# Performance work log

Measured on AMD Instinct MI355X. Metric: run time of the kernel, lower is better.

The kernel has to match this reference:

```python
import jax, jax.numpy as jnp
import numpy as np

PI = np.pi


def _apply_1q(state, gate, wire, n):
    # state: [B, 2**n] complex64; gate: [2,2] (shared) or [B,2,2] (per-sample)
    # PennyLane convention: wire 0 is the most-significant bit of the state index.
    B = state.shape[0]
    left, right = 2 ** wire, 2 ** (n - wire - 1)
    s = state.reshape(B, left, 2, right)
    if gate.ndim == 2:
        s = jnp.einsum('kl,balr->bakr', gate, s)
    else:
        s = jnp.einsum('bkl,balr->bakr', gate, s)
    return s.reshape(B, -1)


def _apply_cz(state, wire, n):
    # CZ on (wire, wire+1): flip sign of |..11..> amplitudes
    B = state.shape[0]
    left, right = 2 ** wire, 2 ** (n - wire - 2)
    s = state.reshape(B, left, 2, 2, right)
    s = s.at[:, :, 1, 1, :].multiply(-1.0)
    return s.reshape(B, -1)


def _ry_batched(theta):
    # theta: [B] -> [B,2,2] complex RY(theta)
    h = 0.5 * theta
    c, s = jnp.cos(h), jnp.sin(h)
    g = jnp.stack([jnp.stack([c, -s], -1), jnp.stack([s, c], -1)], -2)
    return g.astype(jnp.complex64)


def _rot(phi, theta, omega):
    # Rot = RZ(omega) @ RY(theta) @ RZ(phi)
    c, s = jnp.cos(0.5 * theta), jnp.sin(0.5 * theta)
    e_mm = jnp.exp(-0.5j * (phi + omega))
    e_pm = jnp.exp(0.5j * (phi - omega))
    e_mp = jnp.exp(-0.5j * (phi - omega))
    e_pp = jnp.exp(0.5j * (phi + omega))
    g = jnp.stack([jnp.stack([e_mm * c, -e_pm * s]), jnp.stack([e_mp * s, e_pp * c])])
    return g.astype(jnp.complex64)


def _simulate(enc, weights):
    # enc: [B, n_qubits] in [-1,1]; weights: [n_layers, n_qubits, 3]
    n_layers, n, _ = weights.shape
    B = enc.shape[0]
    state = jnp.zeros((B, 2 ** n), jnp.complex64).at[:, 0].set(1.0)
    ry = [_ry_batched(enc[:, i] * PI) for i in range(n)]
    for l in range(n_layers):
        for i in range(n):
            state = _apply_1q(state, ry[i], i, n)
        for i in range(n):
            state = _apply_1q(state, _rot(weights[l, i, 0], weights[l, i, 1], weights[l, i, 2]), i, n)
        for i in range(n - 1):
            state = _apply_cz(state, i, n)
    for i in range(n):
        state = _apply_1q(state, ry[i], i, n)
    probs = state.real ** 2 + state.imag ** 2  # [B, 2**n]
    # <Z_i> = sum_k probs[k] * (-1)^bit_i(k), wire 0 = MSB
    bits = (jnp.arange(2 ** n)[None, :] >> (n - 1 - jnp.arange(n))[:, None]) & 1
    signs = (1 - 2 * bits).astype(probs.dtype)  # [n, 2**n]
    return probs @ signs.T  # [B, n]


def setup_inputs() -> dict:
    B, D, NQ, NL, NA = 32768, 16, 8, 4, 4
    key = jax.random.key(0)
    ks = jax.random.split(key, 6)

    def lin(k, o, i):
        b = 1.0 / np.sqrt(i)
        k1, k2 = jax.random.split(k)
        return (jax.random.uniform(k1, (o, i), jnp.float32, -b, b),
                jax.random.uniform(k2, (o,), jnp.float32, -b, b))

    enc_w1, enc_b1 = lin(ks[1], 8, D)
    enc_w2, enc_b2 = lin(ks[2], NQ, 8)
    dec_w1, dec_b1 = lin(ks[3], 8, NQ)
    dec_w2, dec_b2 = lin(ks[4], NA, 8)
    q_weights = jax.random.uniform(ks[5], (NL, NQ, 3), jnp.float32, 0.0, 2.0 * PI)
    x = jax.random.normal(ks[0], (B, D), jnp.float32)
    return {"x": x, "enc_w1": enc_w1, "enc_b1": enc_b1, "enc_w2": enc_w2, "enc_b2": enc_b2,
            "q_weights": q_weights, "dec_w1": dec_w1, "dec_b1": dec_b1, "dec_w2": dec_w2, "dec_b2": dec_b2}


def reference(x, enc_w1, enc_b1, enc_w2, enc_b2, q_weights, dec_w1, dec_b1, dec_w2, dec_b2):
    h = jax.nn.relu(x @ enc_w1.T + enc_b1)
    enc = jnp.tanh(h @ enc_w2.T + enc_b2)          # [B, n_qubits]
    q = _simulate(enc, q_weights)                  # [B, n_qubits] PauliZ expvals
    h2 = jax.nn.relu(q @ dec_w1.T + dec_b1)
    return h2 @ dec_w2.T + dec_b2                  # [B, n_actions]
```

## Files before the change

### kernel.cpp

```cpp
#include <hip/hip_runtime.h>
#include <math.h>


#define PI_F 3.14159265358979323846f

typedef float v2f __attribute__((ext_vector_type(2)));

struct C2 { float re, im; };
__device__ __forceinline__ C2 cmul(C2 a, C2 b) {
    C2 r;
    r.re = fmaf(a.re, b.re, -a.im * b.im);
    r.im = fmaf(a.re, b.im,  a.im * b.re);
    return r;
}
__device__ __forceinline__ float fxor(float x, int m) {
    return __int_as_float(__float_as_int(x) ^ m);
}

__device__ __forceinline__ v2f pk_fma(v2f a, v2f b, v2f c) {
    v2f d; asm("v_pk_fma_f32 %0, %1, %2, %3" : "=v"(d) : "v"(a), "v"(b), "v"(c)); return d;
}

__device__ __forceinline__ v2f mkbc(float c) { v2f r; r.x = c; return r; }

__device__ __forceinline__ v2f pk_mul_s(float c, v2f z) {
    v2f cb = mkbc(c), d;
    asm("v_pk_mul_f32 %0, %1, %2 op_sel_hi:[0,1]"
        : "=v"(d) : "v"(cb), "v"(z));
    return d;
}
__device__ __forceinline__ v2f pk_mul_neg_s(float c, v2f z) {
    v2f cb = mkbc(c), d;
    asm("v_pk_mul_f32 %0, %1, %2 op_sel_hi:[0,1] neg_lo:[1,0] neg_hi:[1,0]"
        : "=v"(d) : "v"(cb), "v"(z));
    return d;
}
__device__ __forceinline__ v2f pk_fma_s(float c, v2f b, v2f acc) {
    v2f cb = mkbc(c), d;
    asm("v_pk_fma_f32 %0, %1, %2, %3 op_sel_hi:[0,1,1]"
        : "=v"(d) : "v"(cb), "v"(b), "v"(acc));
    return d;
}
__device__ __forceinline__ v2f pk_fma_nn_s(float c, v2f b, v2f acc) {
    v2f cb = mkbc(c), d;
    asm("v_pk_fma_f32 %0, %1, %2, %3 op_sel_hi:[0,1,1] neg_lo:[1,0,0] neg_hi:[1,0,0]"
        : "=v"(d) : "v"(cb), "v"(b), "v"(acc));
    return d;
}
__device__ __forceinline__ v2f pk_fma_swl_s(float c, v2f z, v2f acc) {
    v2f cb = mkbc(c), d;
    asm("v_pk_fma_f32 %0, %1, %2, %3 op_sel:[0,1,0] op_sel_hi:[0,0,1] neg_lo:[1,0,0]"
        : "=v"(d) : "v"(cb), "v"(z), "v"(acc));
    return d;
}
__device__ __forceinline__ v2f pk_fma_swh_s(float c, v2f z, v2f acc) {
    v2f cb = mkbc(c), d;
    asm("v_pk_fma_f32 %0, %1, %2, %3 op_sel:[0,1,0] op_sel_hi:[0,0,1] neg_hi:[1,0,0]"
        : "=v"(d) : "v"(cb), "v"(z), "v"(acc));
    return d;
}
__device__ __forceinline__ v2f cmulv(v2f z, C2 c) {
    return pk_fma_swl_s(c.im, z, pk_mul_s(c.re, z));
}

template<int CTRL>
__device__ __forceinline__ float dppf(float x) {
    int xi = __float_as_int(x);
    int r = __builtin_amdgcn_update_dpp(xi, xi, CTRL, 0xF, 0xF, false);
    return __int_as_float(r);
}
template<int M>
__device__ __forceinline__ float lxor(float x) {
    if constexpr (M == 1)      return dppf<0xB1>(x);
    else if constexpr (M == 2) return dppf<0x4E>(x);
    else                       return dppf<0x128>(x);
}

__device__ __forceinline__ void load_G2(const float* __restrict__ c_lds, int g,
                                        float cc, float ss,
                                        float& ar, float& ai, float& br, float& bi) {
    const float4 c0 = *(const float4*)(c_lds + 4 * g);
    ar = fmaf(c0.x, cc, -c0.z * ss);
    ai = fmaf(c0.y, cc,  c0.w * ss);
    br = fmaf(c0.z, cc,  c0.x * ss);
    bi = fmaf(c0.w, cc, -c0.y * ss);
}

template<int M>
__device__ __forceinline__ void su2_cross(float cSr, float cSi, float cOr, float cOi,
                                          v2f z[32]) {
#pragma unroll
    for (int c = 0; c < 4; c++) {
        v2f p[8];
#pragma unroll
        for (int k = 0; k < 8; k++) {
            p[k].x = lxor<M>(z[c * 8 + k].x);
            p[k].y = lxor<M>(z[c * 8 + k].y);
        }
#pragma unroll
        for (int k = 0; k < 8; k++) {
            const int t = c * 8 + k;
            v2f n = pk_mul_s(cSr, z[t]);
            n = pk_fma_swl_s(cSi, z[t], n);
            n = pk_fma_s    (cOr, p[k], n);
            n = pk_fma_swl_s(cOi, p[k], n);
            z[t] = n;
        }
    }
}

template<int ST>
__device__ __forceinline__ void su2_inlane(float ar, float ai, float br, float bi,
                                           v2f z[32]) {
#pragma unroll
    for (int t = 0; t < 32; t++) {
        if ((t & ST) == 0) {
            const int u = t + ST;
            v2f x = z[t], y = z[u];
            v2f nx = pk_mul_s(ar, x);
            nx = pk_fma_swl_s(ai, x, nx);
            nx = pk_fma_nn_s (br, y, nx);
            nx = pk_fma_swl_s(bi, y, nx);
            v2f ny = pk_mul_s(br, x);
            ny = pk_fma_swl_s(bi, x, ny);
            ny = pk_fma_s    (ar, y, ny);
            ny = pk_fma_swh_s(ai, y, ny);
            z[t] = nx; z[u] = ny;
        }
    }
}

template<int M>
__device__ __forceinline__ v2f xcorr_cross(const v2f z[32]) {
    v2f acc = (v2f){0.0f, 0.0f};
#pragma unroll
    for (int c = 0; c < 4; c++) {
        v2f p[8];
#pragma unroll
        for (int k = 0; k < 8; k++) {
            p[k].x = lxor<M>(z[c * 8 + k].x);
            p[k].y = lxor<M>(z[c * 8 + k].y);
        }
#pragma unroll
        for (int k = 0; k < 8; k++) acc = pk_fma(z[c * 8 + k], p[k], acc);
    }
    return acc;
}
template<int ST>
__device__ __forceinline__ v2f xcorr_inlane(const v2f z[32]) {
    v2f acc = (v2f){0.0f, 0.0f};
#pragma unroll
    for (int t = 0; t < 32; t++)
        if ((t & ST) == 0) acc = pk_fma(z[t], z[t + ST], acc);
    return acc;
}

__host__ __device__ constexpr bool czt5(int t) {
    return ((((t >> 4) & (t >> 3)) ^ ((t >> 3) & (t >> 2)) ^
             ((t >> 2) & (t >> 1)) ^ ((t >> 1) & t)) & 1) != 0;
}

__global__ __launch_bounds__(128, 2) void qdqn_kernel(
    const float* __restrict__ x,
    const float* __restrict__ ew1, const float* __restrict__ eb1,
    const float* __restrict__ ew2, const float* __restrict__ eb2,
    const float* __restrict__ qw,
    const float* __restrict__ dw1, const float* __restrict__ db1,
    const float* __restrict__ dw2, const float* __restrict__ db2,
    float* __restrict__ out, int B, int NL) {
    __shared__ __align__(16) float c_lds[32 * 4];
    __shared__ __align__(16) float hx[2][8][8];
    __shared__ __align__(16) float csx[2][8][16];

    const int tid = threadIdx.x;
    const int wave = tid >> 6;
    const int lane = tid & 63;
    const int g = (lane & 3) | ((lane >> 1) & 4);
    const int grp = ((lane >> 2) & 1) | ((lane >> 3) & 6);
    int s = blockIdx.x * 16 + wave * 8 + grp;
    if (s >= B) s = B - 1;

    float xv[16];
    {
        const float4* xp = (const float4*)(x + s * 16);
#pragma unroll
        for (int i = 0; i < 4; i++) {
            float4 v = xp[i];
            xv[4*i] = v.x; xv[4*i+1] = v.y; xv[4*i+2] = v.z; xv[4*i+3] = v.w;
        }
    }

    const int n_gates = NL * 8;
    if (tid < n_gates) {
        const int gg = tid;
        float phi = qw[3 * gg + 0], th = qw[3 * gg + 1], om = qw[3 * gg + 2];
        float c = __cosf(0.5f * th), sv = __sinf(0.5f * th);
        float A = 0.5f * (phi + om), Bb = 0.5f * (phi - om);
        float* o = c_lds + 4 * gg;
        o[0] =  __cosf(A) * c;   o[1] = -__sinf(A) * c;
        o[2] =  __cosf(Bb) * sv; o[3] = -__sinf(Bb) * sv;
    }
    __syncthreads();

    float cq[8], sq[8];
    {
        float a = eb1[g];
#pragma unroll
        for (int i = 0; i < 16; i++) a = fmaf(ew1[g * 16 + i], xv[i], a);
        hx[wave][grp][g] = fmaxf(a, 0.0f);
        __builtin_amdgcn_wave_barrier();
        float4 h01 = *(const float4*)&hx[wave][grp][0];
        float4 h23 = *(const float4*)&hx[wave][grp][4];
        float b = eb2[g];
        b = fmaf(ew2[g*8+0], h01.x, b); b = fmaf(ew2[g*8+1], h01.y, b);
        b = fmaf(ew2[g*8+2], h01.z, b); b = fmaf(ew2[g*8+3], h01.w, b);
        b = fmaf(ew2[g*8+4], h23.x, b); b = fmaf(ew2[g*8+5], h23.y, b);
        b = fmaf(ew2[g*8+6], h23.z, b); b = fmaf(ew2[g*8+7], h23.w, b);
        float e = 1.0f - __fdividef(2.0f, __expf(2.0f * b) + 1.0f);
        float ang = e * (0.5f * PI_F);
        float2* cso = (float2*)&csx[wave][grp][2 * g];
        *cso = make_float2(__cosf(ang), __sinf(ang));
        __builtin_amdgcn_wave_barrier();
#pragma unroll
        for (int k = 0; k < 4; k++) {
            float4 v = *(const float4*)&csx[wave][grp][4 * k];
            cq[2*k] = v.x; sq[2*k] = v.y; cq[2*k+1] = v.z; sq[2*k+1] = v.w;
        }
    }

    int hiM[3], loM[3];
#pragma unroll
    for (int q = 0; q < 3; q++) {
        int hi = (g >> (2 - q)) & 1;
        hiM[q] = hi << 31;
        loM[q] = hiM[q] ^ 0x80000000;
    }

    const int g0b = g & 1, g1b = (g >> 1) & 1, g2b = (g >> 2) & 1;
    const float mLo = ((g2b & g1b) ^ (g1b & g0b)) ? -1.0f : 1.0f;
    const float mHi = g0b ? -mLo : mLo;

    v2f z[32];
    {
        C2 P; P.re = 1.0f; P.im = 0.0f;
        C2 A[5], Bc[5];
#pragma unroll
        for (int q = 0; q < 8; q++) {
            float ar, ai, br, bi;
            load_G2(c_lds, q, cq[q], sq[q], ar, ai, br, bi);
            if (q < 3) {
                const bool hi = (g >> (2 - q)) & 1;
                C2 f; f.re = hi ? br : ar; f.im = hi ? bi : ai;
                P = cmul(P, f);
            } else {
                A[q-3].re = ar;  A[q-3].im = ai;
                Bc[q-3].re = br; Bc[q-3].im = bi;
            }
        }
        z[0] = (v2f){P.re, P.im};
#pragma unroll
        for (int w = 0; w < 5; w++) {
            const int n = 1 << w;
#pragma unroll
            for (int i = n - 1; i >= 0; i--) {
                v2f v = z[i];
                z[2*i+1] = cmulv(v, Bc[w]);
                z[2*i]   = cmulv(v, A[w]);
            }
        }
#pragma unroll
        for (int t = 0; t < 32; t++) {
            const float m = (t < 16) ? mLo : mHi;
            z[t] = czt5(t) ? pk_mul_neg_s(m, z[t]) : pk_mul_s(m, z[t]);
        }
    }

    for (int l = 1; l < NL; l++) {
        const int gb = l * 8;
        float ar, ai, br, bi;
        load_G2(c_lds, gb+0, cq[0], sq[0], ar, ai, br, bi);
        su2_cross<8>(ar, fxor(ai,hiM[0]), fxor(br,loM[0]), bi, z);
        load_G2(c_lds, gb+1, cq[1], sq[1], ar, ai, br, bi);
        su2_cross<2>(ar, fxor(ai,hiM[1]), fxor(br,loM[1]), bi, z);
        load_G2(c_lds, gb+2, cq[2], sq[2], ar, ai, br, bi);
        su2_cross<1>(ar, fxor(ai,hiM[2]), fxor(br,loM[2]), bi, z);
        load_G2(c_lds, gb+3, cq[3], sq[3], ar, ai, br, bi);
        su2_inlane<16>(ar, ai, br, bi, z);
        load_G2(c_lds, gb+4, cq[4], sq[4], ar, ai, br, bi);
        su2_inlane<8>(ar, ai, br, bi, z);
        load_G2(c_lds, gb+5, cq[5], sq[5], ar, ai, br, bi);
        su2_inlane<4>(ar, ai, br, bi, z);
        load_G2(c_lds, gb+6, cq[6], sq[6], ar, ai, br, bi);
        su2_inlane<2>(ar, ai, br, bi, z);
        load_G2(c_lds, gb+7, cq[7], sq[7], ar, ai, br, bi);
        su2_inlane<1>(ar, ai, br, bi, z);
#pragma unroll
        for (int t = 0; t < 32; t++) {
            const float m = (t < 16) ? mLo : mHi;
            z[t] = czt5(t) ? pk_mul_neg_s(m, z[t]) : pk_mul_s(m, z[t]);
        }
    }

    v2f xa[8];
    xa[0] = xcorr_cross<8>(z);
    xa[1] = xcorr_cross<2>(z);
    xa[2] = xcorr_cross<1>(z);
    xa[3] = xcorr_inlane<16>(z);
    xa[4] = xcorr_inlane<8>(z);
    xa[5] = xcorr_inlane<4>(z);
    xa[6] = xcorr_inlane<2>(z);
    xa[7] = xcorr_inlane<1>(z);

    float p[32];
#pragma unroll
    for (int t = 0; t < 32; t++) p[t] = fmaf(z[t].x, z[t].x, z[t].y * z[t].y);

    float s16[16], zW[8];
    {
        float d = 0.0f;
#pragma unroll
        for (int i = 0; i < 16; i++) {
            s16[i] = p[2*i] + p[2*i+1];
            d += p[2*i] - p[2*i+1];
        }
        zW[7] = d;
        float s8[8]; d = 0.0f;
#pragma unroll
        for (int i = 0; i < 8; i++) {
            s8[i] = s16[2*i] + s16[2*i+1];
            d += s16[2*i] - s16[2*i+1];
        }
        zW[6] = d;
        float s4[4]; d = 0.0f;
#pragma unroll
        for (int i = 0; i < 4; i++) {
            s4[i] = s8[2*i] + s8[2*i+1];
            d += s8[2*i] - s8[2*i+1];
        }
        zW[5] = d;
        float s2a = s4[0] + s4[1], s2b = s4[2] + s4[3];
        zW[4] = (s4[0] - s4[1]) + (s4[2] - s4[3]);
        float sumP = s2a + s2b;
        zW[3] = s2a - s2b;
        zW[0] = g2b ? -sumP : sumP;
        zW[1] = g1b ? -sumP : sumP;
        zW[2] = g0b ? -sumP : sumP;
    }

#pragma unroll
    for (int w = 0; w < 8; w++) {
        const float c2 = fmaf(cq[w], cq[w], -sq[w] * sq[w]);
        const float cs = cq[w] * sq[w];
        const float s2 = (w < 3 ? 2.0f : 4.0f) * cs;
        zW[w] = fmaf(c2, zW[w], -s2 * (xa[w].x + xa[w].y));
    }

#pragma unroll
    for (int w = 0; w < 8; w++) zW[w] += lxor<1>(zW[w]);
#pragma unroll
    for (int w = 0; w < 8; w++) zW[w] += lxor<2>(zW[w]);
#pragma unroll
    for (int w = 0; w < 8; w++) zW[w] += lxor<8>(zW[w]);

    {
        float a = db1[g];
#pragma unroll
        for (int w = 0; w < 8; w++) a = fmaf(dw1[g * 8 + w], zW[w], a);
        hx[wave][grp][g] = fmaxf(a, 0.0f);
        __builtin_amdgcn_wave_barrier();
        float4 h01 = *(const float4*)&hx[wave][grp][0];
        float4 h23 = *(const float4*)&hx[wave][grp][4];
        const int o = g & 3;
        float acc = db2[o];
        acc = fmaf(dw2[o*8+0], h01.x, acc); acc = fmaf(dw2[o*8+1], h01.y, acc);
        acc = fmaf(dw2[o*8+2], h01.z, acc); acc = fmaf(dw2[o*8+3], h01.w, acc);
        acc = fmaf(dw2[o*8+4], h23.x, acc); acc = fmaf(dw2[o*8+5], h23.y, acc);
        acc = fmaf(dw2[o*8+6], h23.z, acc); acc = fmaf(dw2[o*8+7], h23.w, acc);
        out[s * 4 + o] = acc;
    }
}

extern "C" void kernel_launch(void* const* d_in, const int* in_sizes, int n_in,
                              void* d_out, int out_size, void* d_ws, size_t ws_size,
                              hipStream_t stream) {
    const float* x   = (const float*)d_in[0];
    const float* ew1 = (const float*)d_in[1];
    const float* eb1 = (const float*)d_in[2];
    const float* ew2 = (const float*)d_in[3];
    const float* eb2 = (const float*)d_in[4];
    const float* qw  = (const float*)d_in[5];
    const float* dw1 = (const float*)d_in[6];
    const float* db1 = (const float*)d_in[7];
    const float* dw2 = (const float*)d_in[8];
    const float* db2 = (const float*)d_in[9];
    float* out = (float*)d_out;

    int B = in_sizes[0] / 16;
    int n_gates = in_sizes[5] / 3;
    int NL = n_gates / 8;

    int blocks = (B + 15) / 16;
    qdqn_kernel<<<blocks, 128, 0, stream>>>(x, ew1, eb1, ew2, eb2, qw,
                                            dw1, db1, dw2, db2, out, B, NL);
}
```

Before: 116.8 us.

## Use single-wave blocks and batch-load per-layer gate coefficients from LDS

Blocks shrink from two waves to one, with eight samples per block, so the block-wide __syncthreads becomes a wave barrier and the shared arrays lose their wave dimension. Each layer's eight gate coefficient vectors are now read from LDS in one batch before the gate chain, instead of one read right before each gate, so LDS latency can overlap with arithmetic. The grid doubles and each block redoes the trig setup for the gate table, and holding the extra float4s raises register pressure.

```diff
diff --git a/kernel.cpp b/kernel.cpp
--- a/kernel.cpp
+++ b/kernel.cpp
@@ -76,10 +76,8 @@
     else                       return dppf<0x128>(x);
 }
 
-__device__ __forceinline__ void load_G2(const float* __restrict__ c_lds, int g,
-                                        float cc, float ss,
+__device__ __forceinline__ void make_G2(float4 c0, float cc, float ss,
                                         float& ar, float& ai, float& br, float& bi) {
-    const float4 c0 = *(const float4*)(c_lds + 4 * g);
     ar = fmaf(c0.x, cc, -c0.z * ss);
     ai = fmaf(c0.y, cc,  c0.w * ss);
     br = fmaf(c0.z, cc,  c0.x * ss);
@@ -160,7 +158,7 @@
              ((t >> 2) & (t >> 1)) ^ ((t >> 1) & t)) & 1) != 0;
 }
 
-__global__ __launch_bounds__(128, 2) void qdqn_kernel(
+__global__ __launch_bounds__(64, 2) void qdqn_kernel(
     const float* __restrict__ x,
     const float* __restrict__ ew1, const float* __restrict__ eb1,
     const float* __restrict__ ew2, const float* __restrict__ eb2,
@@ -169,15 +167,14 @@
     const float* __restrict__ dw2, const float* __restrict__ db2,
     float* __restrict__ out, int B, int NL) {
     __shared__ __align__(16) float c_lds[32 * 4];
-    __shared__ __align__(16) float hx[2][8][8];
-    __shared__ __align__(16) float csx[2][8][16];
+    __shared__ __align__(16) float hx[8][8];
+    __shared__ __align__(16) float csx[8][16];
 
     const int tid = threadIdx.x;
-    const int wave = tid >> 6;
-    const int lane = tid & 63;
+    const int lane = tid;
     const int g = (lane & 3) | ((lane >> 1) & 4);
     const int grp = ((lane >> 2) & 1) | ((lane >> 3) & 6);
-    int s = blockIdx.x * 16 + wave * 8 + grp;
+    int s = blockIdx.x * 8 + grp;
     if (s >= B) s = B - 1;
 
     float xv[16];
@@ -200,17 +197,17 @@
         o[0] =  __cosf(A) * c;   o[1] = -__sinf(A) * c;
         o[2] =  __cosf(Bb) * sv; o[3] = -__sinf(Bb) * sv;
     }
-    __syncthreads();
+    __builtin_amdgcn_wave_barrier();
 
     float cq[8], sq[8];
     {
         float a = eb1[g];
 #pragma unroll
         for (int i = 0; i < 16; i++) a = fmaf(ew1[g * 16 + i], xv[i], a);
-        hx[wave][grp][g] = fmaxf(a, 0.0f);
+        hx[grp][g] = fmaxf(a, 0.0f);
         __builtin_amdgcn_wave_barrier();
-        float4 h01 = *(const float4*)&hx[wave][grp][0];
-        float4 h23 = *(const float4*)&hx[wave][grp][4];
+        float4 h01 = *(const float4*)&hx[grp][0];
+        float4 h23 = *(const float4*)&hx[grp][4];
         float b = eb2[g];
         b = fmaf(ew2[g*8+0], h01.x, b); b = fmaf(ew2[g*8+1], h01.y, b);
         b = fmaf(ew2[g*8+2], h01.z, b); b = fmaf(ew2[g*8+3], h01.w, b);
@@ -218,12 +215,12 @@
         b = fmaf(ew2[g*8+6], h23.z, b); b = fmaf(ew2[g*8+7], h23.w, b);
         float e = 1.0f - __fdividef(2.0f, __expf(2.0f * b) + 1.0f);
         float ang = e * (0.5f * PI_F);
-        float2* cso = (float2*)&csx[wave][grp][2 * g];
+        float2* cso = (float2*)&csx[grp][2 * g];
         *cso = make_float2(__cosf(ang), __sinf(ang));
         __builtin_amdgcn_wave_barrier();
 #pragma unroll
         for (int k = 0; k < 4; k++) {
-            float4 v = *(const float4*)&csx[wave][grp][4 * k];
+            float4 v = *(const float4*)&csx[grp][4 * k];
             cq[2*k] = v.x; sq[2*k] = v.y; cq[2*k+1] = v.z; sq[2*k+1] = v.w;
         }
     }
@@ -242,12 +239,16 @@
 
     v2f z[32];
     {
+        float4 cA[8];
+#pragma unroll
+        for (int q = 0; q < 8; q++) cA[q] = *(const float4*)(c_lds + 4 * q);
+
         C2 P; P.re = 1.0f; P.im = 0.0f;
         C2 A[5], Bc[5];
 #pragma unroll
         for (int q = 0; q < 8; q++) {
             float ar, ai, br, bi;
-            load_G2(c_lds, q, cq[q], sq[q], ar, ai, br, bi);
+            make_G2(cA[q], cq[q], sq[q], ar, ai, br, bi);
             if (q < 3) {
                 const bool hi = (g >> (2 - q)) & 1;
                 C2 f; f.re = hi ? br : ar; f.im = hi ? bi : ai;
@@ -277,22 +278,26 @@
 
     for (int l = 1; l < NL; l++) {
         const int gb = l * 8;
+        float4 cA[8];
+#pragma unroll
+        for (int q = 0; q < 8; q++) cA[q] = *(const float4*)(c_lds + 4 * (gb + q));
+
         float ar, ai, br, bi;
-        load_G2(c_lds, gb+0, cq[0], sq[0], ar, ai, br, bi);
+        make_G2(cA[0], cq[0], sq[0], ar, ai, br, bi);
         su2_cross<8>(ar, fxor(ai,hiM[0]), fxor(br,loM[0]), bi, z);
-        load_G2(c_lds, gb+1, cq[1], sq[1], ar, ai, br, bi);
+        make_G2(cA[1], cq[1], sq[1], ar, ai, br, bi);
         su2_cross<2>(ar, fxor(ai,hiM[1]), fxor(br,loM[1]), bi, z);
-        load_G2(c_lds, gb+2, cq[2], sq[2], ar, ai, br, bi);
+        make_G2(cA[2], cq[2], sq[2], ar, ai, br, bi);
         su2_cross<1>(ar, fxor(ai,hiM[2]), fxor(br,loM[2]), bi, z);
-        load_G2(c_lds, gb+3, cq[3], sq[3], ar, ai, br, bi);
+        make_G2(cA[3], cq[3], sq[3], ar, ai, br, bi);
         su2_inlane<16>(ar, ai, br, bi, z);
-        load_G2(c_lds, gb+4, cq[4], sq[4], ar, ai, br, bi);
+        make_G2(cA[4], cq[4], sq[4], ar, ai, br, bi);
         su2_inlane<8>(ar, ai, br, bi, z);
-        load_G2(c_lds, gb+5, cq[5], sq[5], ar, ai, br, bi);
+        make_G2(cA[5], cq[5], sq[5], ar, ai, br, bi);
         su2_inlane<4>(ar, ai, br, bi, z);
-        load_G2(c_lds, gb+6, cq[6], sq[6], ar, ai, br, bi);
+        make_G2(cA[6], cq[6], sq[6], ar, ai, br, bi);
         su2_inlane<2>(ar, ai, br, bi, z);
-        load_G2(c_lds, gb+7, cq[7], sq[7], ar, ai, br, bi);
+        make_G2(cA[7], cq[7], sq[7], ar, ai, br, bi);
         su2_inlane<1>(ar, ai, br, bi, z);
 #pragma unroll
         for (int t = 0; t < 32; t++) {
@@ -366,10 +371,10 @@
         float a = db1[g];
 #pragma unroll
         for (int w = 0; w < 8; w++) a = fmaf(dw1[g * 8 + w], zW[w], a);
-        hx[wave][grp][g] = fmaxf(a, 0.0f);
+        hx[grp][g] = fmaxf(a, 0.0f);
         __builtin_amdgcn_wave_barrier();
-        float4 h01 = *(const float4*)&hx[wave][grp][0];
-        float4 h23 = *(const float4*)&hx[wave][grp][4];
+        float4 h01 = *(const float4*)&hx[grp][0];
+        float4 h23 = *(const float4*)&hx[grp][4];
         const int o = g & 3;
         float acc = db2[o];
         acc = fmaf(dw2[o*8+0], h01.x, acc); acc = fmaf(dw2[o*8+1], h01.y, acc);
@@ -399,7 +404,7 @@
     int n_gates = in_sizes[5] / 3;
     int NL = n_gates / 8;
 
-    int blocks = (B + 15) / 16;
-    qdqn_kernel<<<blocks, 128, 0, stream>>>(x, ew1, eb1, ew2, eb2, qw,
-                                            dw1, db1, dw2, db2, out, B, NL);
-}
+    int blocks = (B + 7) / 8;
+    qdqn_kernel<<<blocks, 64, 0, stream>>>(x, ew1, eb1, ew2, eb2, qw,
+                                           dw1, db1, dw2, db2, out, B, NL);
+}
```

Result: no change. 116.0 us (-0.6%).

## Process two samples per wave to interleave independent state-vector updates

Applied to the files above, without the earlier changes.

Each 64-lane wave now simulates two batch samples (A and B) at once instead of one, with blocks shrunk to a single wave and the block barrier replaced by a wave barrier. Gate application, DPP cross-lane exchanges and readouts for both samples are interleaved, giving the scheduler independent instruction streams to hide latency. Weight and gate coefficient loads are also shared between the two samples. The cost is roughly doubled register pressure (two 32-entry complex state arrays), which with launch_bounds(64,1) may reduce occupancy or cause spills.

```diff
diff --git a/kernel.cpp b/kernel.cpp
--- a/kernel.cpp
+++ b/kernel.cpp
@@ -87,8 +87,80 @@
 }
 
 template<int M>
-__device__ __forceinline__ void su2_cross(float cSr, float cSi, float cOr, float cOi,
-                                          v2f z[32]) {
+__device__ __forceinline__ void su2_cross2(
+        float cSrA, float cSiA, float cOrA, float cOiA,
+        float cSrB, float cSiB, float cOrB, float cOiB,
+        v2f zA[32], v2f zB[32]) {
+#pragma unroll
+    for (int c = 0; c < 4; c++) {
+        v2f pA[8], pB[8];
+#pragma unroll
+        for (int k = 0; k < 8; k++) {
+            pA[k].x = lxor<M>(zA[c * 8 + k].x);
+            pA[k].y = lxor<M>(zA[c * 8 + k].y);
+        }
+#pragma unroll
+        for (int k = 0; k < 8; k++) {
+            pB[k].x = lxor<M>(zB[c * 8 + k].x);
+            pB[k].y = lxor<M>(zB[c * 8 + k].y);
+        }
+#pragma unroll
+        for (int k = 0; k < 8; k++) {
+            const int t = c * 8 + k;
+            v2f n = pk_mul_s(cSrA, zA[t]);
+            n = pk_fma_swl_s(cSiA, zA[t], n);
+            n = pk_fma_s    (cOrA, pA[k], n);
+            n = pk_fma_swl_s(cOiA, pA[k], n);
+            zA[t] = n;
+            v2f m = pk_mul_s(cSrB, zB[t]);
+            m = pk_fma_swl_s(cSiB, zB[t], m);
+            m = pk_fma_s    (cOrB, pB[k], m);
+            m = pk_fma_swl_s(cOiB, pB[k], m);
+            zB[t] = m;
+        }
+    }
+}
+
+template<int ST>
+__device__ __forceinline__ void su2_inlane2(
+        float arA, float aiA, float brA, float biA,
+        float arB, float aiB, float brB, float biB,
+        v2f zA[32], v2f zB[32]) {
+#pragma unroll
+    for (int t = 0; t < 32; t++) {
+        if ((t & ST) == 0) {
+            const int u = t + ST;
+            {
+                v2f x = zA[t], y = zA[u];
+                v2f nx = pk_mul_s(arA, x);
+                nx = pk_fma_swl_s(aiA, x, nx);
+                nx = pk_fma_nn_s (brA, y, nx);
+                nx = pk_fma_swl_s(biA, y, nx);
+                v2f ny = pk_mul_s(brA, x);
+                ny = pk_fma_swl_s(biA, x, ny);
+                ny = pk_fma_s    (arA, y, ny);
+                ny = pk_fma_swh_s(aiA, y, ny);
+                zA[t] = nx; zA[u] = ny;
+            }
+            {
+                v2f x = zB[t], y = zB[u];
+                v2f nx = pk_mul_s(arB, x);
+                nx = pk_fma_swl_s(aiB, x, nx);
+                nx = pk_fma_nn_s (brB, y, nx);
+                nx = pk_fma_swl_s(biB, y, nx);
+                v2f ny = pk_mul_s(brB, x);
+                ny = pk_fma_swl_s(biB, x, ny);
+                ny = pk_fma_s    (arB, y, ny);
+                ny = pk_fma_swh_s(aiB, y, ny);
+                zB[t] = nx; zB[u] = ny;
+            }
+        }
+    }
+}
+
+template<int M>
+__device__ __forceinline__ v2f xcorr_cross(const v2f z[32]) {
+    v2f acc = (v2f){0.0f, 0.0f};
 #pragma unroll
     for (int c = 0; c < 4; c++) {
         v2f p[8];
@@ -98,50 +170,6 @@
             p[k].y = lxor<M>(z[c * 8 + k].y);
         }
 #pragma unroll
-        for (int k = 0; k < 8; k++) {
-            const int t = c * 8 + k;
-            v2f n = pk_mul_s(cSr, z[t]);
-            n = pk_fma_swl_s(cSi, z[t], n);
-            n = pk_fma_s    (cOr, p[k], n);
-            n = pk_fma_swl_s(cOi, p[k], n);
-            z[t] = n;
-        }
-    }
-}
-
-template<int ST>
-__device__ __forceinline__ void su2_inlane(float ar, float ai, float br, float bi,
-                                           v2f z[32]) {
-#pragma unroll
-    for (int t = 0; t < 32; t++) {
-        if ((t & ST) == 0) {
-            const int u = t + ST;
-            v2f x = z[t], y = z[u];
-            v2f nx = pk_mul_s(ar, x);
-            nx = pk_fma_swl_s(ai, x, nx);
-            nx = pk_fma_nn_s (br, y, nx);
-            nx = pk_fma_swl_s(bi, y, nx);
-            v2f ny = pk_mul_s(br, x);
-            ny = pk_fma_swl_s(bi, x, ny);
-            ny = pk_fma_s    (ar, y, ny);
-            ny = pk_fma_swh_s(ai, y, ny);
-            z[t] = nx; z[u] = ny;
-        }
-    }
-}
-
-template<int M>
-__device__ __forceinline__ v2f xcorr_cross(const v2f z[32]) {
-    v2f acc = (v2f){0.0f, 0.0f};
-#pragma unroll
-    for (int c = 0; c < 4; c++) {
-        v2f p[8];
-#pragma unroll
-        for (int k = 0; k < 8; k++) {
-            p[k].x = lxor<M>(z[c * 8 + k].x);
-            p[k].y = lxor<M>(z[c * 8 + k].y);
-        }
-#pragma unroll
         for (int k = 0; k < 8; k++) acc = pk_fma(z[c * 8 + k], p[k], acc);
     }
     return acc;
@@ -160,7 +188,43 @@
              ((t >> 2) & (t >> 1)) ^ ((t >> 1) & t)) & 1) != 0;
 }
 
-__global__ __launch_bounds__(128, 2) void qdqn_kernel(
+__device__ __forceinline__ void z_readout(const v2f z[32], int g0b, int g1b, int g2b,
+                                          float zW[8]) {
+    float p[32];
+#pragma unroll
+    for (int t = 0; t < 32; t++) p[t] = fmaf(z[t].x, z[t].x, z[t].y * z[t].y);
+    float s16[16];
+    float d = 0.0f;
+#pragma unroll
+    for (int i = 0; i < 16; i++) {
+        s16[i] = p[2*i] + p[2*i+1];
+        d += p[2*i] - p[2*i+1];
+    }
+    zW[7] = d;
+    float s8[8]; d = 0.0f;
+#pragma unroll
+    for (int i = 0; i < 8; i++) {
+        s8[i] = s16[2*i] + s16[2*i+1];
+        d += s16[2*i] - s16[2*i+1];
+    }
+    zW[6] = d;
+    float s4[4]; d = 0.0f;
+#pragma unroll
+    for (int i = 0; i < 4; i++) {
+        s4[i] = s8[2*i] + s8[2*i+1];
+        d += s8[2*i] - s8[2*i+1];
+    }
+    zW[5] = d;
+    float s2a = s4[0] + s4[1], s2b = s4[2] + s4[3];
+    zW[4] = (s4[0] - s4[1]) + (s4[2] - s4[3]);
+    float sumP = s2a + s2b;
+    zW[3] = s2a - s2b;
+    zW[0] = g2b ? -sumP : sumP;
+    zW[1] = g1b ? -sumP : sumP;
+    zW[2] = g0b ? -sumP : sumP;
+}
+
+__global__ __launch_bounds__(64, 1) void qdqn_kernel(
     const float* __restrict__ x,
     const float* __restrict__ ew1, const float* __restrict__ eb1,
     const float* __restrict__ ew2, const float* __restrict__ eb2,
@@ -169,30 +233,32 @@
     const float* __restrict__ dw2, const float* __restrict__ db2,
     float* __restrict__ out, int B, int NL) {
     __shared__ __align__(16) float c_lds[32 * 4];
-    __shared__ __align__(16) float hx[2][8][8];
-    __shared__ __align__(16) float csx[2][8][16];
-
-    const int tid = threadIdx.x;
-    const int wave = tid >> 6;
-    const int lane = tid & 63;
+    __shared__ __align__(16) float hx[16][8];
+    __shared__ __align__(16) float csx[16][16];
+
+    const int lane = threadIdx.x;
     const int g = (lane & 3) | ((lane >> 1) & 4);
     const int grp = ((lane >> 2) & 1) | ((lane >> 3) & 6);
-    int s = blockIdx.x * 16 + wave * 8 + grp;
-    if (s >= B) s = B - 1;
-
-    float xv[16];
+    int sA = blockIdx.x * 16 + grp;
+    int sB = sA + 8;
+    if (sA >= B) sA = B - 1;
+    if (sB >= B) sB = B - 1;
+
+    float xvA[16], xvB[16];
     {
-        const float4* xp = (const float4*)(x + s * 16);
+        const float4* xpA = (const float4*)(x + sA * 16);
+        const float4* xpB = (const float4*)(x + sB * 16);
 #pragma unroll
         for (int i = 0; i < 4; i++) {
-            float4 v = xp[i];
-            xv[4*i] = v.x; xv[4*i+1] = v.y; xv[4*i+2] = v.z; xv[4*i+3] = v.w;
+            float4 a = xpA[i], b = xpB[i];
+            xvA[4*i] = a.x; xvA[4*i+1] = a.y; xvA[4*i+2] = a.z; xvA[4*i+3] = a.w;
+            xvB[4*i] = b.x; xvB[4*i+1] = b.y; xvB[4*i+2] = b.z; xvB[4*i+3] = b.w;
         }
     }
 
     const int n_gates = NL * 8;
-    if (tid < n_gates) {
-        const int gg = tid;
+    if (lane < n_gates) {
+        const int gg = lane;
         float phi = qw[3 * gg + 0], th = qw[3 * gg + 1], om = qw[3 * gg + 2];
         float c = __cosf(0.5f * th), sv = __sinf(0.5f * th);
         float A = 0.5f * (phi + om), Bb = 0.5f * (phi - om);
@@ -200,31 +266,50 @@
         o[0] =  __cosf(A) * c;   o[1] = -__sinf(A) * c;
         o[2] =  __cosf(Bb) * sv; o[3] = -__sinf(Bb) * sv;
     }
-    __syncthreads();
-
-    float cq[8], sq[8];
+    __builtin_amdgcn_wave_barrier();
+
+    float cqA[8], sqA[8], cqB[8], sqB[8];
     {
-        float a = eb1[g];
-#pragma unroll
-        for (int i = 0; i < 16; i++) a = fmaf(ew1[g * 16 + i], xv[i], a);
-        hx[wave][grp][g] = fmaxf(a, 0.0f);
+        float w1[16];
+#pragma unroll
+        for (int i = 0; i < 16; i++) w1[i] = ew1[g * 16 + i];
+        float aA = eb1[g], aB = aA;
+#pragma unroll
+        for (int i = 0; i < 16; i++) {
+            aA = fmaf(w1[i], xvA[i], aA);
+            aB = fmaf(w1[i], xvB[i], aB);
+        }
+        hx[grp][g]     = fmaxf(aA, 0.0f);
+        hx[grp + 8][g] = fmaxf(aB, 0.0f);
         __builtin_amdgcn_wave_barrier();
-        float4 h01 = *(const float4*)&hx[wave][grp][0];
-        float4 h23 = *(const float4*)&hx[wave][grp][4];
-        float b = eb2[g];
-        b = fmaf(ew2[g*8+0], h01.x, b); b = fmaf(ew2[g*8+1], h01.y, b);
-        b = fmaf(ew2[g*8+2], h01.z, b); b = fmaf(ew2[g*8+3], h01.w, b);
-        b = fmaf(ew2[g*8+4], h23.x, b); b = fmaf(ew2[g*8+5], h23.y, b);
-        b = fmaf(ew2[g*8+6], h23.z, b); b = fmaf(ew2[g*8+7], h23.w, b);
-        float e = 1.0f - __fdividef(2.0f, __expf(2.0f * b) + 1.0f);
-        float ang = e * (0.5f * PI_F);
-        float2* cso = (float2*)&csx[wave][grp][2 * g];
-        *cso = make_float2(__cosf(ang), __sinf(ang));
+        float4 hA01 = *(const float4*)&hx[grp][0];
+        float4 hA23 = *(const float4*)&hx[grp][4];
+        float4 hB01 = *(const float4*)&hx[grp + 8][0];
+        float4 hB23 = *(const float4*)&hx[grp + 8][4];
+        float w2[8];
+#pragma unroll
+        for (int i = 0; i < 8; i++) w2[i] = ew2[g * 8 + i];
+        float bA = eb2[g], bB = bA;
+        bA = fmaf(w2[0], hA01.x, bA); bB = fmaf(w2[0], hB01.x, bB);
+        bA = fmaf(w2[1], hA01.y, bA); bB = fmaf(w2[1], hB01.y, bB);
+        bA = fmaf(w2[2], hA01.z, bA); bB = fmaf(w2[2], hB01.z, bB);
+        bA = fmaf(w2[3], hA01.w, bA); bB = fmaf(w2[3], hB01.w, bB);
+        bA = fmaf(w2[4], hA23.x, bA); bB = fmaf(w2[4], hB23.x, bB);
+        bA = fmaf(w2[5], hA23.y, bA); bB = fmaf(w2[5], hB23.y, bB);
+        bA = fmaf(w2[6], hA23.z, bA); bB = fmaf(w2[6], hB23.z, bB);
+        bA = fmaf(w2[7], hA23.w, bA); bB = fmaf(w2[7], hB23.w, bB);
+        float eA = 1.0f - __fdividef(2.0f, __expf(2.0f * bA) + 1.0f);
+        float eB = 1.0f - __fdividef(2.0f, __expf(2.0f * bB) + 1.0f);
+        float angA = eA * (0.5f * PI_F), angB = eB * (0.5f * PI_F);
+        *(float2*)&csx[grp][2 * g]     = make_float2(__cosf(angA), __sinf(angA));
+        *(float2*)&csx[grp + 8][2 * g] = make_float2(__cosf(angB), __sinf(angB));
         __builtin_amdgcn_wave_barrier();
 #pragma unroll
         for (int k = 0; k < 4; k++) {
-            float4 v = *(const float4*)&csx[wave][grp][4 * k];
-            cq[2*k] = v.x; sq[2*k] = v.y; cq[2*k+1] = v.z; sq[2*k+1] = v.w;
+            float4 a = *(const float4*)&csx[grp][4 * k];
+            float4 b = *(const float4*)&csx[grp + 8][4 * k];
+            cqA[2*k] = a.x; sqA[2*k] = a.y; cqA[2*k+1] = a.z; sqA[2*k+1] = a.w;
+            cqB[2*k] = b.x; sqB[2*k] = b.y; cqB[2*k+1] = b.z; sqB[2*k+1] = b.w;
         }
     }
 
@@ -240,143 +325,163 @@
     const float mLo = ((g2b & g1b) ^ (g1b & g0b)) ? -1.0f : 1.0f;
     const float mHi = g0b ? -mLo : mLo;
 
-    v2f z[32];
+    v2f zA[32], zB[32];
     {
-        C2 P; P.re = 1.0f; P.im = 0.0f;
-        C2 A[5], Bc[5];
+        C2 PA; PA.re = 1.0f; PA.im = 0.0f;
+        C2 PB = PA;
+        C2 AA[5], BcA[5], AB[5], BcB[5];
 #pragma unroll
         for (int q = 0; q < 8; q++) {
             float ar, ai, br, bi;
-            load_G2(c_lds, q, cq[q], sq[q], ar, ai, br, bi);
+            load_G2(c_lds, q, cqA[q], sqA[q], ar, ai, br, bi);
+            float arB_, aiB_, brB_, biB_;
+            load_G2(c_lds, q, cqB[q], sqB[q], arB_, aiB_, brB_, biB_);
             if (q < 3) {
                 const bool hi = (g >> (2 - q)) & 1;
-                C2 f; f.re = hi ? br : ar; f.im = hi ? bi : ai;
-                P = cmul(P, f);
+                C2 fA; fA.re = hi ? br : ar;   fA.im = hi ? bi : ai;
+                C2 fB; fB.re = hi ? brB_ : arB_; fB.im = hi ? biB_ : aiB_;
+                PA = cmul(PA, fA);
+                PB = cmul(PB, fB);
             } else {
-                A[q-3].re = ar;  A[q-3].im = ai;
-                Bc[q-3].re = br; Bc[q-3].im = bi;
+                AA[q-3].re = ar;    AA[q-3].im = ai;
+                BcA[q-3].re = br;   BcA[q-3].im = bi;
+                AB[q-3].re = arB_;  AB[q-3].im = aiB_;
+                BcB[q-3].re = brB_; BcB[q-3].im = biB_;
             }
         }
-        z[0] = (v2f){P.re, P.im};
+        zA[0] = (v2f){PA.re, PA.im};
+        zB[0] = (v2f){PB.re, PB.im};
 #pragma unroll
         for (int w = 0; w < 5; w++) {
             const int n = 1 << w;
 #pragma unroll
             for (int i = n - 1; i >= 0; i--) {
-                v2f v = z[i];
-                z[2*i+1] = cmulv(v, Bc[w]);
-                z[2*i]   = cmulv(v, A[w]);
+                v2f vA = zA[i], vB = zB[i];
+                zA[2*i+1] = cmulv(vA, BcA[w]);
+                zA[2*i]   = cmulv(vA, AA[w]);
+                zB[2*i+1] = cmulv(vB, BcB[w]);
+                zB[2*i]   = cmulv(vB, AB[w]);
             }
         }
 #pragma unroll
         for (int t = 0; t < 32; t++) {
             const float m = (t < 16) ? mLo : mHi;
-            z[t] = czt5(t) ? pk_mul_neg_s(m, z[t]) : pk_mul_s(m, z[t]);
+            zA[t] = czt5(t) ? pk_mul_neg_s(m, zA[t]) : pk_mul_s(m, zA[t]);
+            zB[t] = czt5(t) ? pk_mul_neg_s(m, zB[t]) : pk_mul_s(m, zB[t]);
         }
     }
 
     for (int l = 1; l < NL; l++) {
         const int gb = l * 8;
-        float ar, ai, br, bi;
-        load_G2(c_lds, gb+0, cq[0], sq[0], ar, ai, br, bi);
-        su2_cross<8>(ar, fxor(ai,hiM[0]), fxor(br,loM[0]), bi, z);
-        load_G2(c_lds, gb+1, cq[1], sq[1], ar, ai, br, bi);
-        su2_cross<2>(ar, fxor(ai,hiM[1]), fxor(br,loM[1]), bi, z);
-        load_G2(c_lds, gb+2, cq[2], sq[2], ar, ai, br, bi);
-        su2_cross<1>(ar, fxor(ai,hiM[2]), fxor(br,loM[2]), bi, z);
-        load_G2(c_lds, gb+3, cq[3], sq[3], ar, ai, br, bi);
-        su2_inlane<16>(ar, ai, br, bi, z);
-        load_G2(c_lds, gb+4, cq[4], sq[4], ar, ai, br, bi);
-        su2_inlane<8>(ar, ai, br, bi, z);
-        load_G2(c_lds, gb+5, cq[5], sq[5], ar, ai, br, bi);
-        su2_inlane<4>(ar, ai, br, bi, z);
-        load_G2(c_lds, gb+6, cq[6], sq[6], ar, ai, br, bi);
-        su2_inlane<2>(ar, ai, br, bi, z);
-        load_G2(c_lds, gb+7, cq[7], sq[7], ar, ai, br, bi);
-        su2_inlane<1>(ar, ai, br, bi, z);
+        float ar, ai, br, bi, arB_, aiB_, brB_, biB_;
+
+        load_G2(c_lds, gb+0, cqA[0], sqA[0], ar, ai, br, bi);
+        load_G2(c_lds, gb+0, cqB[0], sqB[0], arB_, aiB_, brB_, biB_);
+        su2_cross2<8>(ar, fxor(ai,hiM[0]), fxor(br,loM[0]), bi,
+                      arB_, fxor(aiB_,hiM[0]), fxor(brB_,loM[0]), biB_, zA, zB);
+
+        load_G2(c_lds, gb+1, cqA[1], sqA[1], ar, ai, br, bi);
+        load_G2(c_lds, gb+1, cqB[1], sqB[1], arB_, aiB_, brB_, biB_);
+        su2_cross2<2>(ar, fxor(ai,hiM[1]), fxor(br,loM[1]), bi,
+                      arB_, fxor(aiB_,hiM[1]), fxor(brB_,loM[1]), biB_, zA, zB);
+
+        load_G2(c_lds, gb+2, cqA[2], sqA[2], ar, ai, br, bi);
+        load_G2(c_lds, gb+2, cqB[2], sqB[2], arB_, aiB_, brB_, biB_);
+        su2_cross2<1>(ar, fxor(ai,hiM[2]), fxor(br,loM[2]), bi,
+                      arB_, fxor(aiB_,hiM[2]), fxor(brB_,loM[2]), biB_, zA, zB);
+
+        load_G2(c_lds, gb+3, cqA[3], sqA[3], ar, ai, br, bi);
+        load_G2(c_lds, gb+3, cqB[3], sqB[3], arB_, aiB_, brB_, biB_);
+        su2_inlane2<16>(ar, ai, br, bi, arB_, aiB_, brB_, biB_, zA, zB);
+
+        load_G2(c_lds, gb+4, cqA[4], sqA[4], ar, ai, br, bi);
+        load_G2(c_lds, gb+4, cqB[4], sqB[4], arB_, aiB_, brB_, biB_);
+        su2_inlane2<8>(ar, ai, br, bi, arB_, aiB_, brB_, biB_, zA, zB);
+
+        load_G2(c_lds, gb+5, cqA[5], sqA[5], ar, ai, br, bi);
+        load_G2(c_lds, gb+5, cqB[5], sqB[5], arB_, aiB_, brB_, biB_);
+        su2_inlane2<4>(ar, ai, br, bi, arB_, aiB_, brB_, biB_, zA, zB);
+
+        load_G2(c_lds, gb+6, cqA[6], sqA[6], ar, ai, br, bi);
+        load_G2(c_lds, gb+6, cqB[6], sqB[6], arB_, aiB_, brB_, biB_);
+        su2_inlane2<2>(ar, ai, br, bi, arB_, aiB_, brB_, biB_, zA, zB);
+
+        load_G2(c_lds, gb+7, cqA[7], sqA[7], ar, ai, br, bi);
+        load_G2(c_lds, gb+7, cqB[7], sqB[7], arB_, aiB_, brB_, biB_);
+        su2_inlane2<1>(ar, ai, br, bi, arB_, aiB_, brB_, biB_, zA, zB);
+
 #pragma unroll
         for (int t = 0; t < 32; t++) {
             const float m = (t < 16) ? mLo : mHi;
-            z[t] = czt5(t) ? pk_mul_neg_s(m, z[t]) : pk_mul_s(m, z[t]);
-        }
-    }
-
-    v2f xa[8];
-    xa[0] = xcorr_cross<8>(z);
-    xa[1] = xcorr_cross<2>(z);
-    xa[2] = xcorr_cross<1>(z);
-    xa[3] = xcorr_inlane<16>(z);
-    xa[4] = xcorr_inlane<8>(z);
-    xa[5] = xcorr_inlane<4>(z);
-    xa[6] = xcorr_inlane<2>(z);
-    xa[7] = xcorr_inlane<1>(z);
-
-    float p[32];
-#pragma unroll
-    for (int t = 0; t < 32; t++) p[t] = fmaf(z[t].x, z[t].x, z[t].y * z[t].y);
-
-    float s16[16], zW[8];
+            zA[t] = czt5(t) ? pk_mul_neg_s(m, zA[t]) : pk_mul_s(m, zA[t]);
+            zB[t] = czt5(t) ? pk_mul_neg_s(m, zB[t]) : pk_mul_s(m, zB[t]);
+        }
+    }
+
+    v2f xaA[8], xaB[8];
+    xaA[0] = xcorr_cross<8>(zA);  xaB[0] = xcorr_cross<8>(zB);
+    xaA[1] = xcorr_cross<2>(zA);  xaB[1] = xcorr_cross<2>(zB);
+    xaA[2] = xcorr_cross<1>(zA);  xaB[2] = xcorr_cross<1>(zB);
+    xaA[3] = xcorr_inlane<16>(zA); xaB[3] = xcorr_inlane<16>(zB);
+    xaA[4] = xcorr_inlane<8>(zA);  xaB[4] = xcorr_inlane<8>(zB);
+    xaA[5] = xcorr_inlane<4>(zA);  xaB[5] = xcorr_inlane<4>(zB);
+    xaA[6] = xcorr_inlane<2>(zA);  xaB[6] = xcorr_inlane<2>(zB);
+    xaA[7] = xcorr_inlane<1>(zA);  xaB[7] = xcorr_inlane<1>(zB);
+
+    float zWA[8], zWB[8];
+    z_readout(zA, g0b, g1b, g2b, zWA);
+    z_readout(zB, g0b, g1b, g2b, zWB);
+
+#pragma unroll
+    for (int w = 0; w < 8; w++) {
+        const float fac = (w < 3 ? 2.0f : 4.0f);
+        const float c2A = fmaf(cqA[w], cqA[w], -sqA[w] * sqA[w]);
+        const float s2A = fac * (cqA[w] * sqA[w]);
+        zWA[w] = fmaf(c2A, zWA[w], -s2A * (xaA[w].x + xaA[w].y));
+        const float c2B = fmaf(cqB[w], cqB[w], -sqB[w] * sqB[w]);
+        const float s2B = fac * (cqB[w] * sqB[w]);
+        zWB[w] = fmaf(c2B, zWB[w], -s2B * (xaB[w].x + xaB[w].y));
+    }
+
+#pragma unroll
+    for (int w = 0; w < 8; w++) { zWA[w] += lxor<1>(zWA[w]); zWB[w] += lxor<1>(zWB[w]); }
+#pragma unroll
+    for (int w = 0; w < 8; w++) { zWA[w] += lxor<2>(zWA[w]); zWB[w] += lxor<2>(zWB[w]); }
+#pragma unroll
+    for (int w = 0; w < 8; w++) { zWA[w] += lxor<8>(zWA[w]); zWB[w] += lxor<8>(zWB[w]); }
+
     {
-        float d = 0.0f;
-#pragma unroll
-        for (int i = 0; i < 16; i++) {
-            s16[i] = p[2*i] + p[2*i+1];
-            d += p[2*i] - p[2*i+1];
-        }
-        zW[7] = d;
-        float s8[8]; d = 0.0f;
-#pragma unroll
-        for (int i = 0; i < 8; i++) {
-            s8[i] = s16[2*i] + s16[2*i+1];
-            d += s16[2*i] - s16[2*i+1];
-        }
-        zW[6] = d;
-        float s4[4]; d = 0.0f;
-#pragma unroll
-        for (int i = 0; i < 4; i++) {
-            s4[i] = s8[2*i] + s8[2*i+1];
-            d += s8[2*i] - s8[2*i+1];
-        }
-        zW[5] = d;
-        float s2a = s4[0] + s4[1], s2b = s4[2] + s4[3];
-        zW[4] = (s4[0] - s4[1]) + (s4[2] - s4[3]);
-        float sumP = s2a + s2b;
-        zW[3] = s2a - s2b;
-        zW[0] = g2b ? -sumP : sumP;
-        zW[1] = g1b ? -sumP : sumP;
-        zW[2] = g0b ? -sumP : sumP;
-    }
-
-#pragma unroll
-    for (int w = 0; w < 8; w++) {
-        const float c2 = fmaf(cq[w], cq[w], -sq[w] * sq[w]);
-        const float cs = cq[w] * sq[w];
-        const float s2 = (w < 3 ? 2.0f : 4.0f) * cs;
-        zW[w] = fmaf(c2, zW[w], -s2 * (xa[w].x + xa[w].y));
-    }
-
-#pragma unroll
-    for (int w = 0; w < 8; w++) zW[w] += lxor<1>(zW[w]);
-#pragma unroll
-    for (int w = 0; w < 8; w++) zW[w] += lxor<2>(zW[w]);
-#pragma unroll
-    for (int w = 0; w < 8; w++) zW[w] += lxor<8>(zW[w]);
-
-    {
-        float a = db1[g];
-#pragma unroll
-        for (int w = 0; w < 8; w++) a = fmaf(dw1[g * 8 + w], zW[w], a);
-        hx[wave][grp][g] = fmaxf(a, 0.0f);
+        float d1[8];
+#pragma unroll
+        for (int w = 0; w < 8; w++) d1[w] = dw1[g * 8 + w];
+        float aA = db1[g], aB = aA;
+#pragma unroll
+        for (int w = 0; w < 8; w++) {
+            aA = fmaf(d1[w], zWA[w], aA);
+            aB = fmaf(d1[w], zWB[w], aB);
+        }
+        hx[grp][g]     = fmaxf(aA, 0.0f);
+        hx[grp + 8][g] = fmaxf(aB, 0.0f);
         __builtin_amdgcn_wave_barrier();
-        float4 h01 = *(const float4*)&hx[wave][grp][0];
-        float4 h23 = *(const float4*)&hx[wave][grp][4];
+        float4 hA01 = *(const float4*)&hx[grp][0];
+        float4 hA23 = *(const float4*)&hx[grp][4];
+        float4 hB01 = *(const float4*)&hx[grp + 8][0];
+        float4 hB23 = *(const float4*)&hx[grp + 8][4];
         const int o = g & 3;
-        float acc = db2[o];
-        acc = fmaf(dw2[o*8+0], h01.x, acc); acc = fmaf(dw2[o*8+1], h01.y, acc);
-        acc = fmaf(dw2[o*8+2], h01.z, acc); acc = fmaf(dw2[o*8+3], h01.w, acc);
-        acc = fmaf(dw2[o*8+4], h23.x, acc); acc = fmaf(dw2[o*8+5], h23.y, acc);
-        acc = fmaf(dw2[o*8+6], h23.z, acc); acc = fmaf(dw2[o*8+7], h23.w, acc);
-        out[s * 4 + o] = acc;
+        float d2[8];
+#pragma unroll
+        for (int i = 0; i < 8; i++) d2[i] = dw2[o * 8 + i];
+        float accA = db2[o], accB = accA;
+        accA = fmaf(d2[0], hA01.x, accA); accB = fmaf(d2[0], hB01.x, accB);
+        accA = fmaf(d2[1], hA01.y, accA); accB = fmaf(d2[1], hB01.y, accB);
+        accA = fmaf(d2[2], hA01.z, accA); accB = fmaf(d2[2], hB01.z, accB);
+        accA = fmaf(d2[3], hA01.w, accA); accB = fmaf(d2[3], hB01.w, accB);
+        accA = fmaf(d2[4], hA23.x, accA); accB = fmaf(d2[4], hB23.x, accB);
+        accA = fmaf(d2[5], hA23.y, accA); accB = fmaf(d2[5], hB23.y, accB);
+        accA = fmaf(d2[6], hA23.z, accA); accB = fmaf(d2[6], hB23.z, accB);
+        accA = fmaf(d2[7], hA23.w, accA); accB = fmaf(d2[7], hB23.w, accB);
+        out[sA * 4 + o] = accA;
+        out[sB * 4 + o] = accB;
     }
 }
 
@@ -400,6 +505,6 @@
     int NL = n_gates / 8;
 
     int blocks = (B + 15) / 16;
-    qdqn_kernel<<<blocks, 128, 0, stream>>>(x, ew1, eb1, ew2, eb2, qw,
-                                            dw1, db1, dw2, db2, out, B, NL);
-}
+    qdqn_kernel<<<blocks, 64, 0, stream>>>(x, ew1, eb1, ew2, eb2, qw,
+                                           dw1, db1, dw2, db2, out, B, NL);
+}
```

After: 115.4 us, median of 2. No clear change (-1.2%).
